# Kernel optimization log

Measured on AMD Instinct MI355X. Metric: run time of the kernel, lower is better.

## Reference

```python
import jax, jax.numpy as jnp
import numpy as np

B, T, C, H = 4, 2048, 1024, 16

def setup_inputs() -> dict:
    key = jax.random.key(0)
    k1, k2, k3, k4, k5 = jax.random.split(key, 5)
    s = 1.0 / np.sqrt(C)
    return {
        "x": jax.random.normal(k1, (B, T, C), dtype=jnp.float32),
        "w_attn": jax.random.normal(k2, (C, 3 * C), dtype=jnp.float32) * s,
        "b_attn": jax.random.normal(k3, (3 * C,), dtype=jnp.float32) * 0.02,
        "w_proj": jax.random.normal(k4, (C, C), dtype=jnp.float32) * s,
        "b_proj": jax.random.normal(k5, (C,), dtype=jnp.float32) * 0.02,
    }

def reference(x, w_attn, b_attn, w_proj, b_proj):
    Bx, Tx, Cx = x.shape
    hd = Cx // H  # head_size
    qkv = x @ w_attn + b_attn                      # [B,T,3C]
    q, k, v = jnp.split(qkv, 3, axis=2)
    # [B,T,C] -> [B,H,T,hd]
    def heads(t):
        return t.reshape(Bx, Tx, H, hd).transpose(0, 2, 1, 3)
    q, k, v = heads(q), heads(k), heads(v)
    scale = hd ** -0.5
    scores = jnp.einsum("bhqd,bhkd->bhqk", q, k) * scale  # [B,H,T,T]
    causal = jnp.tril(jnp.ones((Tx, Tx), dtype=bool))
    scores = jnp.where(causal[None, None], scores, -jnp.inf)
    probs = jax.nn.softmax(scores, axis=-1)
    attn = jnp.einsum("bhqk,bhkd->bhqd", probs, v)  # [B,H,T,hd]
    attn = attn.transpose(0, 2, 1, 3).reshape(Bx, Tx, Cx)
    return attn @ w_proj + b_proj
```

## Files before the change

### kernel.cpp

```cpp
#include <hip/hip_runtime.h>
#include <hip/hip_bf16.h>

#define BATCH 4
#define TSEQ  2048
#define CDIM  1024
#define NHEAD 16
#define HDIM  64
#define C3    3072
#define MROWS (BATCH * TSEQ)

#define QSCALE 0.18033688011112f

typedef short bf16x8 __attribute__((ext_vector_type(8)));
typedef short short8 __attribute__((ext_vector_type(8)));
typedef __bf16 bf16v8 __attribute__((ext_vector_type(8)));
typedef float f32x4 __attribute__((ext_vector_type(4)));
typedef unsigned int u32x4v __attribute__((ext_vector_type(4)));

#define AS1 __attribute__((address_space(1)))
#define AS3 __attribute__((address_space(3)))

#if __has_builtin(__builtin_amdgcn_exp2f)
#define EXP2F(x) __builtin_amdgcn_exp2f(x)
#else
#define EXP2F(x) exp2f(x)
#endif

__device__ __forceinline__ short f2bf(float x) {
    unsigned int u = __builtin_bit_cast(unsigned int, x);
    u += 0x7fffu + ((u >> 16) & 1u);
    return (short)(u >> 16);
}

__device__ __forceinline__ unsigned int cvtpk(float lo, float hi) {
    unsigned int r;
    asm("v_cvt_pk_bf16_f32 %0, %1, %2" : "=v"(r) : "v"(lo), "v"(hi));
    return r;
}

__device__ __forceinline__ f32x4 mfma16(bf16x8 a, bf16x8 b, f32x4 c) {
    return __builtin_amdgcn_mfma_f32_16x16x32_bf16(
        __builtin_bit_cast(bf16v8, a), __builtin_bit_cast(bf16v8, b), c, 0, 0, 0);
}

__device__ __forceinline__ void vpack_write(short* dst, const bf16x8& r0,
                                            const bf16x8& r1, int skv, int sd0) {
#if __has_builtin(__builtin_amdgcn_perm)
    u32x4v a = __builtin_bit_cast(u32x4v, r0);
    u32x4v b = __builtin_bit_cast(u32x4v, r1);
#pragma unroll
    for (int wd = 0; wd < 4; ++wd) {
        unsigned int lo = __builtin_amdgcn_perm(b[wd], a[wd], 0x05040100u);
        unsigned int hi = __builtin_amdgcn_perm(b[wd], a[wd], 0x07060302u);
        *(unsigned int*)&dst[(sd0 + 2 * wd + 0) * 72 + skv] = lo;
        *(unsigned int*)&dst[(sd0 + 2 * wd + 1) * 72 + skv] = hi;
    }
#else
#pragma unroll
    for (int i = 0; i < 8; ++i) {
        unsigned int pk = (unsigned short)r0[i] | ((unsigned int)(unsigned short)r1[i] << 16);
        *(unsigned int*)&dst[(sd0 + i) * 72 + skv] = pk;
    }
#endif
}

__global__ void prep_kernel(const float* __restrict__ x, short* __restrict__ x_bf,
                            const float* __restrict__ wA, short* __restrict__ wAT,
                            const float* __restrict__ wP, short* __restrict__ wPT,
                            float qs) {
    const int tx = threadIdx.x, ty = threadIdx.y;
    if (blockIdx.z == 0) {
        const int i = (blockIdx.y * 128 + blockIdx.x) * 256 + ty * 32 + tx;
        float4 a = ((const float4*)x)[2 * i];
        float4 b = ((const float4*)x)[2 * i + 1];
        short8 o;
        o[0] = f2bf(a.x); o[1] = f2bf(a.y); o[2] = f2bf(a.z); o[3] = f2bf(a.w);
        o[4] = f2bf(b.x); o[5] = f2bf(b.y); o[6] = f2bf(b.z); o[7] = f2bf(b.w);
        ((short8*)x_bf)[i] = o;
        return;
    }
    const float* in;
    short* out;
    int N, qcols;
    float sc;
    if (blockIdx.z == 1) {
        if (blockIdx.x >= C3 / 32) return;
        in = wA; out = wAT; N = C3; qcols = CDIM; sc = qs;
    } else {
        if (blockIdx.x >= CDIM / 32) return;
        in = wP; out = wPT; N = CDIM; qcols = 0; sc = 1.0f;
    }
    __shared__ float tile[32][33];
    const int n0 = blockIdx.x * 32, k0 = blockIdx.y * 32;
#pragma unroll
    for (int j = 0; j < 4; ++j)
        tile[ty + j * 8][tx] = in[(size_t)(k0 + ty + j * 8) * N + n0 + tx];
    __syncthreads();
#pragma unroll
    for (int j = 0; j < 4; ++j) {
        const int n = n0 + ty + j * 8;
        const float s = (n < qcols) ? sc : 1.0f;
        out[(size_t)n * CDIM + k0 + tx] = f2bf(tile[tx][ty + j * 8] * s);
    }
}

template <typename OutT, int WAVES_M, int WAVES_N, int BN>
__global__ __launch_bounds__(512, 4) void gemm3_kernel(
    const short* __restrict__ A, const short* __restrict__ Bt,
    const float* __restrict__ bias, OutT* __restrict__ out,
    int M, int N, int K, int qcols, float qs) {
    constexpr int BM = 128;
    constexpr int MF = BM / (WAVES_M * 16);
    constexpr int NF = BN / (WAVES_N * 16);
    constexpr int BLOADS = BN / 128;
    __shared__ alignas(16) short Ab[3][BM * 32];
    __shared__ alignas(16) short Bb[3][BN * 32];

    const int tid = threadIdx.x;
    const int lane = tid & 63;
    const int w = tid >> 6;
    const int wm = w / WAVES_N;
    const int wn = w % WAVES_N;

    const int nwg = gridDim.x * gridDim.y;
    const int lid = blockIdx.y * gridDim.x + blockIdx.x;
    const int swz = (lid & 7) * (nwg >> 3) + (lid >> 3);
    const int m0 = (swz / gridDim.x) * BM;
    const int n0 = (swz % gridDim.x) * BN;

    const int NT = K >> 5;

    const int fr = lane & 15;
    const int ch = lane >> 4;

    f32x4 acc[MF][NF] = {};

    const int rA  = tid >> 2;
    const int lcA = (tid & 3) ^ ((rA >> 1) & 3);
    const short* gA = A + (size_t)(m0 + rA) * K + lcA * 8;
    const short* gB[BLOADS];
#pragma unroll
    for (int i = 0; i < BLOADS; ++i) {
        const int s = tid + i * 512;
        const int r = s >> 2;
        const int lc = (s & 3) ^ ((r >> 1) & 3);
        gB[i] = Bt + (size_t)(n0 + r) * K + lc * 8;
    }

    int aoff[MF], boff[NF];
#pragma unroll
    for (int f = 0; f < MF; ++f) {
        const int r = wm * (BM / WAVES_M) + f * 16 + fr;
        aoff[f] = r * 32 + (ch ^ ((r >> 1) & 3)) * 8;
    }
#pragma unroll
    for (int f = 0; f < NF; ++f) {
        const int r = wn * (BN / WAVES_N) + f * 16 + fr;
        boff[f] = r * 32 + (ch ^ ((r >> 1) & 3)) * 8;
    }

#define GSTAGE(buf, kt)                                                          \
    do {                                                                         \
        __builtin_amdgcn_global_load_lds((const AS1 void*)(gA + (kt)),           \
            (AS3 void*)&Ab[buf][w * 512], 16, 0, 0);                             \
        _Pragma("unroll")                                                        \
        for (int i = 0; i < BLOADS; ++i)                                         \
            __builtin_amdgcn_global_load_lds((const AS1 void*)(gB[i] + (kt)),    \
                (AS3 void*)&Bb[buf][i * 4096 + w * 512], 16, 0, 0);              \
    } while (0)

#define GITER(BUF, T)                                                            \
    do {                                                                         \
        if constexpr (BLOADS == 2) {                                             \
            asm volatile("s_waitcnt vmcnt(3)" ::: "memory");                     \
        } else {                                                                 \
            asm volatile("s_waitcnt vmcnt(2)" ::: "memory");                     \
        }                                                                        \
        __builtin_amdgcn_s_barrier();                                            \
        const int ktn = (((T) + 2 < NT) ? ((T) + 2) : 0) * 32;                   \
        GSTAGE((BUF + 2) % 3, ktn);                                              \
        __builtin_amdgcn_sched_barrier(0);                                       \
        bf16x8 af[MF], bfv[NF];                                                  \
        _Pragma("unroll")                                                        \
        for (int f = 0; f < MF; ++f)                                             \
            af[f] = *(const bf16x8*)&Ab[BUF][aoff[f]];                           \
        _Pragma("unroll")                                                        \
        for (int f = 0; f < NF; ++f)                                             \
            bfv[f] = *(const bf16x8*)&Bb[BUF][boff[f]];                          \
        _Pragma("unroll")                                                        \
        for (int mf = 0; mf < MF; ++mf)                                          \
            _Pragma("unroll")                                                    \
            for (int nf = 0; nf < NF; ++nf)                                      \
                acc[mf][nf] = mfma16(af[mf], bfv[nf], acc[mf][nf]);              \
    } while (0)

    GSTAGE(0, 0);
    GSTAGE(1, 32);

    int t = 0;
    for (; t + 3 <= NT; t += 3) {
        GITER(0, t);
        GITER(1, t + 1);
        GITER(2, t + 2);
    }
    if (t < NT) { GITER(0, t); ++t; }
    if (t < NT) { GITER(1, t); }
#undef GITER
#undef GSTAGE

    const int r0 = (lane >> 4) * 4;
    const int cn = lane & 15;
#pragma unroll
    for (int mf = 0; mf < MF; ++mf) {
#pragma unroll
        for (int nf = 0; nf < NF; ++nf) {
            const int col = n0 + wn * (BN / WAVES_N) + nf * 16 + cn;
            const float bv = bias[col] * ((col < qcols) ? qs : 1.0f);
#pragma unroll
            for (int r = 0; r < 4; ++r) {
                const int row = m0 + wm * (BM / WAVES_M) + mf * 16 + r0 + r;
                const float v = acc[mf][nf][r] + bv;
                if constexpr (sizeof(OutT) == 2)
                    out[(size_t)row * N + col] = (OutT)f2bf(v);
                else
                    out[(size_t)row * N + col] = (OutT)v;
            }
        }
    }
}

template <int BUF>
__device__ __forceinline__ void attn_iter(
    int KB, int niter, int qrow, int w, int cn, int g, int kg8,
    int krow, int kx0, int kx1, int skv, int sd0,
    const short* kgl, size_t ksrc, const short* vbase,
    short (*klds)[64 * 64], short (*vt)[64 * 72],
    const bf16x8 (&qf)[2][2], f32x4 (&ao)[2][4], f32x4 (&ao4)[2],
    const bf16x8& vones) {

    const int kvb = KB * 64;
    const bool pf = (KB + 1 < niter);

    bf16x8 r0, r1;
    if (pf) {
        r0 = *(const bf16x8*)(vbase + (size_t)(kvb + 64 + skv) * C3 + sd0);
        r1 = *(const bf16x8*)(vbase + (size_t)(kvb + 64 + skv + 1) * C3 + sd0);
        const short* kn = kgl + ksrc + (size_t)(kvb + 64) * C3;
        __builtin_amdgcn_global_load_lds((const AS1 void*)kn,
            (AS3 void*)&klds[BUF ^ 1][w * 512], 16, 0, 0);
        __builtin_amdgcn_global_load_lds((const AS1 void*)(kn + (size_t)32 * C3),
            (AS3 void*)&klds[BUF ^ 1][2048 + w * 512], 16, 0, 0);
    }

    if (kvb <= qrow + 31) {
        bf16x8 kf[4][2];
#pragma unroll
        for (int t = 0; t < 4; ++t) {
            const int rb = t * 1024 + krow;
            kf[t][0] = *(const bf16x8*)&klds[BUF][rb + kx0];
            kf[t][1] = *(const bf16x8*)&klds[BUF][rb + kx1];
        }

        bf16x8 vf[2][4];
#pragma unroll
        for (int c = 0; c < 2; ++c)
#pragma unroll
            for (int dt = 0; dt < 4; ++dt)
                vf[c][dt] = *(const bf16x8*)&vt[BUF][(dt * 16 + cn) * 72 + c * 32 + kg8];

#pragma unroll
        for (int qt = 0; qt < 2; ++qt) {
            const int qrow16 = qrow + qt * 16;

            f32x4 s[4] = {};
#pragma unroll
            for (int t = 0; t < 4; ++t) {
                s[t] = mfma16(kf[t][0], qf[qt][0], s[t]);
                s[t] = mfma16(kf[t][1], qf[qt][1], s[t]);
            }

            const bool maskIter = (kvb + 63 > qrow16);
            float p[4][4];
            if (maskIter) {
#pragma unroll
                for (int t = 0; t < 4; ++t)
#pragma unroll
                    for (int r = 0; r < 4; ++r) {
                        const int kv = kvb + t * 16 + 4 * g + r;
                        const int q  = qrow16 + cn;
                        float e = EXP2F(s[t][r]);
                        p[t][r] = (kv > q) ? 0.f : e;
                    }
            } else {
#pragma unroll
                for (int t = 0; t < 4; ++t)
#pragma unroll
                    for (int r = 0; r < 4; ++r)
                        p[t][r] = EXP2F(s[t][r]);
            }

            unsigned int wq[8];
#pragma unroll
            for (int t = 0; t < 4; ++t) {
                wq[t * 2 + 0] = cvtpk(p[t][0], p[t][1]);
                wq[t * 2 + 1] = cvtpk(p[t][2], p[t][3]);
            }

#pragma unroll
            for (int c = 0; c < 2; ++c) {
                union { unsigned int u[4]; bf16x8 v; } pu;
                unsigned int p0 = wq[4 * c + 0], p2 = wq[4 * c + 2];
                asm("v_permlane32_swap_b32 %0, %1" : "+v"(p0), "+v"(p2));
                asm("v_permlane16_swap_b32 %0, %1" : "+v"(p0), "+v"(p2));
                pu.u[0] = p0; pu.u[2] = p2;
                unsigned int p1 = wq[4 * c + 1], p3 = wq[4 * c + 3];
                asm("v_permlane32_swap_b32 %0, %1" : "+v"(p1), "+v"(p3));
                asm("v_permlane16_swap_b32 %0, %1" : "+v"(p1), "+v"(p3));
                pu.u[1] = p1; pu.u[3] = p3;
#pragma unroll
                for (int dt = 0; dt < 4; ++dt)
                    ao[qt][dt] = mfma16(pu.v, vf[c][dt], ao[qt][dt]);
                ao4[qt] = mfma16(pu.v, vones, ao4[qt]);
            }
        }
    }

    if (pf) vpack_write(vt[BUF ^ 1], r0, r1, skv, sd0);
    __syncthreads();
}

__global__ __launch_bounds__(256) void attn_kernel(const short* __restrict__ qkv,
                                                   short* __restrict__ attn_out) {
    __shared__ short vt[2][64 * 72];
    __shared__ short klds[2][64 * 64];

    const int tid = threadIdx.x;
    const int lane = tid & 63;
    const int w = tid >> 6;

    const int bid = blockIdx.x;
    const int swz = (bid & 7) * 64 + (bid >> 3);
    const int bh = swz >> 3;
    const int pairp = swz & 7;
    const int b = bh >> 4;
    const int h = bh & 15;

    const size_t base = (size_t)b * TSEQ * C3 + (size_t)h * HDIM;
    const int cn = lane & 15;
    const int g = lane >> 4;
    const int kg8 = g * 8;

    const bf16x8 vones = {0x3F80, 0x3F80, 0x3F80, 0x3F80,
                          0x3F80, 0x3F80, 0x3F80, 0x3F80};

    const short* kgl = qkv + base + 1024;
    const size_t ksrc = (size_t)(w * 8 + (lane >> 3)) * C3 + ((lane & 7) ^ (lane >> 3)) * 8;
    const int cnl = cn & 7;
    const int krow = cn * 64;
    const int kx0 = ((g ^ cnl) * 8);
    const int kx1 = (((g ^ 4) ^ cnl) * 8);

    const int skv = (tid & 31) * 2;
    const int sd0 = (tid >> 5) * 8;
    const short* vbase = qkv + base + 2048;

    for (int pass = 0; pass < 2; ++pass) {
        const int qi = pass ? pairp : (15 - pairp);
        const int q0 = qi * 128;
        const int qrow = q0 + w * 32;
        const int niter = 2 * qi + 2;

        bf16x8 qf[2][2];
#pragma unroll
        for (int qt = 0; qt < 2; ++qt)
#pragma unroll
            for (int ks = 0; ks < 2; ++ks)
                qf[qt][ks] = *(const bf16x8*)(qkv + base +
                    (size_t)(qrow + qt * 16 + cn) * C3 + ks * 32 + kg8);

        f32x4 ao[2][4] = {};
        f32x4 ao4[2] = {};

        {
            __builtin_amdgcn_global_load_lds((const AS1 void*)(kgl + ksrc),
                                             (AS3 void*)&klds[0][w * 512], 16, 0, 0);
            __builtin_amdgcn_global_load_lds((const AS1 void*)(kgl + ksrc + (size_t)32 * C3),
                                             (AS3 void*)&klds[0][2048 + w * 512], 16, 0, 0);
            bf16x8 r0 = *(const bf16x8*)(vbase + (size_t)skv * C3 + sd0);
            bf16x8 r1 = *(const bf16x8*)(vbase + (size_t)(skv + 1) * C3 + sd0);
            vpack_write(vt[0], r0, r1, skv, sd0);
        }
        __syncthreads();

        int kb = 0;
        for (; kb + 2 <= niter; kb += 2) {
            attn_iter<0>(kb,     niter, qrow, w, cn, g, kg8, krow, kx0, kx1,
                         skv, sd0, kgl, ksrc, vbase, klds, vt, qf, ao, ao4, vones);
            attn_iter<1>(kb + 1, niter, qrow, w, cn, g, kg8, krow, kx0, kx1,
                         skv, sd0, kgl, ksrc, vbase, klds, vt, qf, ao, ao4, vones);
        }

#pragma unroll
        for (int qt = 0; qt < 2; ++qt) {
#pragma unroll
            for (int r = 0; r < 4; ++r) {
                const float lr = 1.0f / ao4[qt][r];
                const int q = qrow + qt * 16 + 4 * g + r;
#pragma unroll
                for (int dt = 0; dt < 4; ++dt)
                    attn_out[(size_t)(b * TSEQ + q) * CDIM + h * HDIM + dt * 16 + cn] =
                        f2bf(ao[qt][dt][r] * lr);
            }
        }
        __syncthreads();
    }
}

extern "C" void kernel_launch(void* const* d_in, const int* in_sizes, int n_in,
                              void* d_out, int out_size, void* d_ws, size_t ws_size,
                              hipStream_t stream) {
    const float* x      = (const float*)d_in[0];
    const float* w_attn = (const float*)d_in[1];
    const float* b_attn = (const float*)d_in[2];
    const float* w_proj = (const float*)d_in[3];
    const float* b_proj = (const float*)d_in[4];
    float* out = (float*)d_out;

    char* ws = (char*)d_ws;
    short* x_bf   = (short*)ws;
    short* wqkvT  = (short*)(ws + (16u << 20));
    short* wprojT = (short*)(ws + (22u << 20));
    short* qkv    = (short*)(ws + (24u << 20));

    prep_kernel<<<dim3(128, 32, 3), dim3(32, 8), 0, stream>>>(
        x, x_bf, w_attn, wqkvT, w_proj, wprojT, QSCALE);

    gemm3_kernel<short, 2, 4, 256><<<dim3(C3 / 256, MROWS / 128), 512, 0, stream>>>(
        x_bf, wqkvT, b_attn, qkv, MROWS, C3, CDIM, CDIM, QSCALE);

    attn_kernel<<<dim3(512), 256, 0, stream>>>(qkv, x_bf);

    gemm3_kernel<float, 4, 2, 128><<<dim3(CDIM / 128, MROWS / 128), 512, 0, stream>>>(
        x_bf, wprojT, b_proj, out, MROWS, CDIM, CDIM, 0, 1.0f);
}
```

Measured before the change: 158.1 us.

## Load K fragments directly from global into registers, drop K LDS staging

K tiles are no longer staged through shared memory with global_load_lds. Each wave now loads its own K MFMA fragments straight from global memory into double-buffered registers, and skips the prefetch when the next block is fully masked. The full __syncthreads at the end of each iteration becomes an LDS-only waitcnt plus s_barrier, so pending global K loads can stay in flight across the barrier. The cost is that each of the four waves fetches the full K tile separately, which quadruples K global/L2 traffic, and the extra fragment registers raise register pressure.

```diff
diff --git a/kernel.cpp b/kernel.cpp
--- a/kernel.cpp
+++ b/kernel.cpp
@@ -231,10 +231,11 @@
 
 template <int BUF>
 __device__ __forceinline__ void attn_iter(
-    int KB, int niter, int qrow, int w, int cn, int g, int kg8,
-    int krow, int kx0, int kx1, int skv, int sd0,
-    const short* kgl, size_t ksrc, const short* vbase,
-    short (*klds)[64 * 64], short (*vt)[64 * 72],
+    int KB, int niter, int qrow, int cn, int g, int kg8,
+    int skv, int sd0,
+    const short* kgl, const short* vbase,
+    short (*vt)[64 * 72],
+    const bf16x8 (&kfc)[4][2], bf16x8 (&kfn)[4][2],
     const bf16x8 (&qf)[2][2], f32x4 (&ao)[2][4], f32x4 (&ao4)[2],
     const bf16x8& vones) {
 
@@ -245,22 +246,17 @@
     if (pf) {
         r0 = *(const bf16x8*)(vbase + (size_t)(kvb + 64 + skv) * C3 + sd0);
         r1 = *(const bf16x8*)(vbase + (size_t)(kvb + 64 + skv + 1) * C3 + sd0);
-        const short* kn = kgl + ksrc + (size_t)(kvb + 64) * C3;
-        __builtin_amdgcn_global_load_lds((const AS1 void*)kn,
-            (AS3 void*)&klds[BUF ^ 1][w * 512], 16, 0, 0);
-        __builtin_amdgcn_global_load_lds((const AS1 void*)(kn + (size_t)32 * C3),
-            (AS3 void*)&klds[BUF ^ 1][2048 + w * 512], 16, 0, 0);
+    }
+    if (pf && (kvb + 64 <= qrow + 31)) {
+        const short* kn = kgl + (size_t)(kvb + 64 + cn) * C3 + kg8;
+#pragma unroll
+        for (int t = 0; t < 4; ++t) {
+            kfn[t][0] = *(const bf16x8*)(kn + (size_t)(t * 16) * C3);
+            kfn[t][1] = *(const bf16x8*)(kn + (size_t)(t * 16) * C3 + 32);
+        }
     }
 
     if (kvb <= qrow + 31) {
-        bf16x8 kf[4][2];
-#pragma unroll
-        for (int t = 0; t < 4; ++t) {
-            const int rb = t * 1024 + krow;
-            kf[t][0] = *(const bf16x8*)&klds[BUF][rb + kx0];
-            kf[t][1] = *(const bf16x8*)&klds[BUF][rb + kx1];
-        }
-
         bf16x8 vf[2][4];
 #pragma unroll
         for (int c = 0; c < 2; ++c)
@@ -275,8 +271,8 @@
             f32x4 s[4] = {};
 #pragma unroll
             for (int t = 0; t < 4; ++t) {
-                s[t] = mfma16(kf[t][0], qf[qt][0], s[t]);
-                s[t] = mfma16(kf[t][1], qf[qt][1], s[t]);
+                s[t] = mfma16(kfc[t][0], qf[qt][0], s[t]);
+                s[t] = mfma16(kfc[t][1], qf[qt][1], s[t]);
             }
 
             const bool maskIter = (kvb + 63 > qrow16);
@@ -326,13 +322,13 @@
     }
 
     if (pf) vpack_write(vt[BUF ^ 1], r0, r1, skv, sd0);
-    __syncthreads();
+    asm volatile("s_waitcnt lgkmcnt(0)" ::: "memory");
+    __builtin_amdgcn_s_barrier();
 }
 
 __global__ __launch_bounds__(256) void attn_kernel(const short* __restrict__ qkv,
                                                    short* __restrict__ attn_out) {
     __shared__ short vt[2][64 * 72];
-    __shared__ short klds[2][64 * 64];
 
     const int tid = threadIdx.x;
     const int lane = tid & 63;
@@ -354,12 +350,6 @@
                           0x3F80, 0x3F80, 0x3F80, 0x3F80};
 
     const short* kgl = qkv + base + 1024;
-    const size_t ksrc = (size_t)(w * 8 + (lane >> 3)) * C3 + ((lane & 7) ^ (lane >> 3)) * 8;
-    const int cnl = cn & 7;
-    const int krow = cn * 64;
-    const int kx0 = ((g ^ cnl) * 8);
-    const int kx1 = (((g ^ 4) ^ cnl) * 8);
-
     const int skv = (tid & 31) * 2;
     const int sd0 = (tid >> 5) * 8;
     const short* vbase = qkv + base + 2048;
@@ -380,12 +370,15 @@
 
         f32x4 ao[2][4] = {};
         f32x4 ao4[2] = {};
+        bf16x8 kfA[4][2], kfB[4][2];
 
         {
-            __builtin_amdgcn_global_load_lds((const AS1 void*)(kgl + ksrc),
-                                             (AS3 void*)&klds[0][w * 512], 16, 0, 0);
-            __builtin_amdgcn_global_load_lds((const AS1 void*)(kgl + ksrc + (size_t)32 * C3),
-                                             (AS3 void*)&klds[0][2048 + w * 512], 16, 0, 0);
+            const short* kp = kgl + (size_t)cn * C3 + kg8;
+#pragma unroll
+            for (int t = 0; t < 4; ++t) {
+                kfA[t][0] = *(const bf16x8*)(kp + (size_t)(t * 16) * C3);
+                kfA[t][1] = *(const bf16x8*)(kp + (size_t)(t * 16) * C3 + 32);
+            }
             bf16x8 r0 = *(const bf16x8*)(vbase + (size_t)skv * C3 + sd0);
             bf16x8 r1 = *(const bf16x8*)(vbase + (size_t)(skv + 1) * C3 + sd0);
             vpack_write(vt[0], r0, r1, skv, sd0);
@@ -394,10 +387,10 @@
 
         int kb = 0;
         for (; kb + 2 <= niter; kb += 2) {
-            attn_iter<0>(kb,     niter, qrow, w, cn, g, kg8, krow, kx0, kx1,
-                         skv, sd0, kgl, ksrc, vbase, klds, vt, qf, ao, ao4, vones);
-            attn_iter<1>(kb + 1, niter, qrow, w, cn, g, kg8, krow, kx0, kx1,
-                         skv, sd0, kgl, ksrc, vbase, klds, vt, qf, ao, ao4, vones);
+            attn_iter<0>(kb,     niter, qrow, cn, g, kg8, skv, sd0,
+                         kgl, vbase, vt, kfA, kfB, qf, ao, ao4, vones);
+            attn_iter<1>(kb + 1, niter, qrow, cn, g, kg8, skv, sd0,
+                         kgl, vbase, vt, kfB, kfA, qf, ao, ao4, vones);
         }
 
 #pragma unroll
```

Result: slower. 209.4 us (+32.4%).
